# Kernel optimization log

Measured on AMD Instinct MI355X. Metric: run time of the kernel, lower is better.

Reference implementation:

```python
import jax, jax.numpy as jnp
import numpy as np

K = 3
NUM_STEP_COMBO = 5
BN_EPS = 1e-5


def setup_inputs() -> dict:
    key = jax.random.key(0)
    ks = jax.random.split(key, 10)
    N, E, D, H, O, G = 100000, 1600000, 48, 128, 12, 64
    x = jax.random.normal(ks[0], (N, D), dtype=jnp.float32)
    edge_index = jax.random.randint(ks[1], (2, E), 0, N, dtype=jnp.int64)
    batch = jnp.sort(jax.random.randint(ks[2], (N,), 0, G, dtype=jnp.int64))
    # ChebConv params: one [D, D] weight per Chebyshev order, shared bias
    W = jax.random.normal(ks[3], (K, D, D), dtype=jnp.float32) * 0.1
    b = jnp.zeros((D,), dtype=jnp.float32)
    gamma = jnp.ones((D,), dtype=jnp.float32)
    beta = jnp.zeros((D,), dtype=jnp.float32)
    W1 = jax.random.normal(ks[4], (D, H), dtype=jnp.float32) * 0.1
    b1 = jnp.zeros((H,), dtype=jnp.float32)
    W2 = jax.random.normal(ks[5], (H, O), dtype=jnp.float32) * 0.1
    b2 = jnp.zeros((O,), dtype=jnp.float32)
    return {"x": x, "edge_index": edge_index, "batch": batch, "num_graphs": 64,
            "W": W, "b": b, "gamma": gamma, "beta": beta,
            "W1": W1, "b1": b1, "W2": W2, "b2": b2}


def cheb_conv(x, row, col, W, b):
    # PyG ChebConv, sym norm, lambda_max=2 => L_hat = -D^{-1/2} A D^{-1/2}
    N = x.shape[0]
    deg = jax.ops.segment_sum(jnp.ones_like(row, dtype=x.dtype), row, num_segments=N)
    dinv = jnp.where(deg > 0, jax.lax.rsqrt(jnp.maximum(deg, 1.0)), 0.0)
    norm = (-dinv[row] * dinv[col])[:, None]  # [E,1] edge weights of L_hat

    def lhat(v):  # sparse matvec: gather neighbors, scale, scatter-add
        return jax.ops.segment_sum(norm * v[col], row, num_segments=N)

    Tx0 = x
    Tx1 = lhat(x)
    out = Tx0 @ W[0] + Tx1 @ W[1]
    Txkm2, Txkm1 = Tx0, Tx1
    for k in range(2, W.shape[0]):
        Txk = 2.0 * lhat(Txkm1) - Txkm2
        out = out + Txk @ W[k]
        Txkm2, Txkm1 = Txkm1, Txk
    return out + b


def reference(x, edge_index, batch, num_graphs, W, b, gamma, beta, W1, b1, W2, b2):
    row, col = edge_index[0], edge_index[1]
    N = x.shape[0]
    out = x
    for _ in range(NUM_STEP_COMBO):
        t = jax.nn.relu(cheb_conv(out, row, col, W, b))
        # BatchNorm1d (training-mode stats over all nodes, biased var)
        mean = jnp.mean(t, axis=0)
        var = jnp.mean((t - mean) ** 2, axis=0)
        t = gamma * (t - mean) * jax.lax.rsqrt(var + BN_EPS) + beta
        # graph_max_pool: per-node max over incoming neighbor features
        m = jax.ops.segment_max(t[col], row, num_segments=N)
        out = jnp.where(jnp.isneginf(m), 0.0, m)  # empty segments -> 0
    g = jax.ops.segment_sum(out, batch, num_segments=num_graphs)  # global_add_pool
    h = jax.nn.relu(g @ W1 + b1)
    return h @ W2 + b2
```

## Files before the change

kernel.cpp:

```cpp
#include <hip/hip_runtime.h>
#include <hip/hip_bf16.h>

#define D 48
#define GNUM 64
#define HDIM 128
#define ODIM 12
#define BN_EPS 1e-5f

typedef _Float16 half2v __attribute__((ext_vector_type(2)));
typedef _Float16 half4v __attribute__((ext_vector_type(4)));
typedef _Float16 half8v __attribute__((ext_vector_type(8)));

#if __has_builtin(__builtin_amdgcn_fdot2)
#define FDOT2(a, b, c) __builtin_amdgcn_fdot2((a), (b), (c), false)
#else
#define FDOT2(a, b, c) ((c) + (float)(a)[0] * (float)(b)[0] + (float)(a)[1] * (float)(b)[1])
#endif


__global__ __launch_bounds__(256) void k_deg(const int* __restrict__ row, int* __restrict__ deg, int E) {
    int e = blockIdx.x * 256 + threadIdx.x;
    if (e < E) atomicAdd(&deg[row[e]], 1);
}

__global__ __launch_bounds__(256) void k_dinv(const int* __restrict__ deg, float* __restrict__ dinv, int N) {
    int i = blockIdx.x * 256 + threadIdx.x;
    if (i < N) dinv[i] = deg[i] > 0 ? rsqrtf((float)deg[i]) : 0.f;
}

__global__ __launch_bounds__(256) void k_scan1(const int* __restrict__ deg, int* __restrict__ incl,
                                               int* __restrict__ bsum, int N) {
    __shared__ int s[256];
    int i = blockIdx.x * 256 + threadIdx.x;
    s[threadIdx.x] = (i < N) ? deg[i] : 0;
    __syncthreads();
    for (int off = 1; off < 256; off <<= 1) {
        int t = (threadIdx.x >= off) ? s[threadIdx.x - off] : 0;
        __syncthreads();
        s[threadIdx.x] += t;
        __syncthreads();
    }
    if (i < N) incl[i] = s[threadIdx.x];
    if (threadIdx.x == 255) bsum[blockIdx.x] = s[255];
}

__global__ __launch_bounds__(512) void k_scan2(int* __restrict__ bsum, int nb) {
    __shared__ int s[512];
    int t = threadIdx.x;
    s[t] = (t < nb) ? bsum[t] : 0;
    __syncthreads();
    for (int off = 1; off < 512; off <<= 1) {
        int v = (t >= off) ? s[t - off] : 0;
        __syncthreads();
        s[t] += v;
        __syncthreads();
    }
    if (t < nb) bsum[t] = s[t];
}

__global__ __launch_bounds__(256) void k_scan3(const int* __restrict__ incl, const int* __restrict__ bsum,
                                               int* __restrict__ rowptr, int N) {
    int i = blockIdx.x * 256 + threadIdx.x;
    if (i < N) {
        int add = (blockIdx.x > 0) ? bsum[blockIdx.x - 1] : 0;
        rowptr[i + 1] = incl[i] + add;
    }
    if (i == 0) rowptr[0] = 0;
}

__global__ __launch_bounds__(256) void k_fill(const int* __restrict__ row, const int* __restrict__ col,
                                              const int* __restrict__ rowptr, int* __restrict__ fillc,
                                              int* __restrict__ ecol, int E) {
    int e = blockIdx.x * 256 + threadIdx.x;
    if (e < E) {
        int r = row[e], c = col[e];
        int p = rowptr[r] + atomicAdd(&fillc[r], 1);
        ecol[p] = c;
    }
}

__global__ __launch_bounds__(256) void k_cvt(const float* __restrict__ x, const float* __restrict__ dinv,
                                             _Float16* __restrict__ xh, _Float16* __restrict__ xs, int n4) {
    int i = blockIdx.x * 256 + threadIdx.x;
    if (i < n4) {
        int node = i / 12;
        float dv = dinv[node];
        float4 v = ((const float4*)x)[i];
        half4v h, hs;
        h.x = (_Float16)v.x; h.y = (_Float16)v.y; h.z = (_Float16)v.z; h.w = (_Float16)v.w;
        hs.x = (_Float16)(dv * v.x); hs.y = (_Float16)(dv * v.y);
        hs.z = (_Float16)(dv * v.z); hs.w = (_Float16)(dv * v.w);
        ((half4v*)xh)[i] = h;
        ((half4v*)xs)[i] = hs;
    }
}


__global__ __launch_bounds__(256) void k_lhat(const _Float16* __restrict__ curs, const int* __restrict__ rowptr,
                                              const int* __restrict__ ecol, const float* __restrict__ dinv,
                                              _Float16* __restrict__ tx1, _Float16* __restrict__ tx1s, int N) {
    int lane = threadIdx.x & 63;
    int i = (blockIdx.x * 256 + threadIdx.x) >> 6;
    if (i >= N) return;
    int q = lane & 7, slot = lane >> 3;
    int qc = q < 6 ? q : 5;
    int s = rowptr[i], e = rowptr[i + 1];
    float a[8] = {0.f, 0.f, 0.f, 0.f, 0.f, 0.f, 0.f, 0.f};
    int p = s + slot;
    for (; p + 8 < e; p += 16) {
        int ca = ecol[p], cb = ecol[p + 8];
        half8v ha = *(const half8v*)(curs + (size_t)ca * D + qc * 8);
        half8v hb = *(const half8v*)(curs + (size_t)cb * D + qc * 8);
#pragma unroll
        for (int j = 0; j < 8; ++j) a[j] += (float)ha[j] + (float)hb[j];
    }
    if (p < e) {
        int ca = ecol[p];
        half8v ha = *(const half8v*)(curs + (size_t)ca * D + qc * 8);
#pragma unroll
        for (int j = 0; j < 8; ++j) a[j] += (float)ha[j];
    }
#pragma unroll
    for (int j = 0; j < 8; ++j) {
        a[j] += __shfl_xor(a[j], 8);
        a[j] += __shfl_xor(a[j], 16);
        a[j] += __shfl_xor(a[j], 32);
    }
    if (lane < 6) {
        float di = dinv[i];
        half8v o, os;
#pragma unroll
        for (int j = 0; j < 8; ++j) {
            float t = -di * a[j];
            o[j] = (_Float16)t;
            os[j] = (_Float16)(di * t);
        }
        *(half8v*)(tx1 + (size_t)i * D + lane * 8) = o;
        *(half8v*)(tx1s + (size_t)i * D + lane * 8) = os;
    }
}

__global__ __launch_bounds__(256) void k_gather2(const _Float16* __restrict__ tx0, const _Float16* __restrict__ tx1s,
                                                 const int* __restrict__ rowptr, const int* __restrict__ ecol,
                                                 const float* __restrict__ dinv, _Float16* __restrict__ tx2, int N) {
    int lane = threadIdx.x & 63;
    int i = (blockIdx.x * 256 + threadIdx.x) >> 6;
    if (i >= N) return;
    int q = lane & 7, slot = lane >> 3;
    int qc = q < 6 ? q : 5;
    int s = rowptr[i], e = rowptr[i + 1];
    float a[8] = {0.f, 0.f, 0.f, 0.f, 0.f, 0.f, 0.f, 0.f};
    int p = s + slot;
    for (; p + 8 < e; p += 16) {
        int ca = ecol[p], cb = ecol[p + 8];
        half8v ha = *(const half8v*)(tx1s + (size_t)ca * D + qc * 8);
        half8v hb = *(const half8v*)(tx1s + (size_t)cb * D + qc * 8);
#pragma unroll
        for (int j = 0; j < 8; ++j) a[j] += (float)ha[j] + (float)hb[j];
    }
    if (p < e) {
        int ca = ecol[p];
        half8v ha = *(const half8v*)(tx1s + (size_t)ca * D + qc * 8);
#pragma unroll
        for (int j = 0; j < 8; ++j) a[j] += (float)ha[j];
    }
#pragma unroll
    for (int j = 0; j < 8; ++j) {
        a[j] += __shfl_xor(a[j], 8);
        a[j] += __shfl_xor(a[j], 16);
        a[j] += __shfl_xor(a[j], 32);
    }
    if (lane < 6) {
        float sc = -2.f * dinv[i];
        half8v h0 = *(const half8v*)(tx0 + (size_t)i * D + lane * 8);
        half8v o;
#pragma unroll
        for (int j = 0; j < 8; ++j) o[j] = (_Float16)(sc * a[j] - (float)h0[j]);
        *(half8v*)(tx2 + (size_t)i * D + lane * 8) = o;
    }
}


__global__ __launch_bounds__(256) void k_dense(const _Float16* __restrict__ tx0, const _Float16* __restrict__ tx1,
                                               const _Float16* __restrict__ tx2, const float* __restrict__ W,
                                               const float* __restrict__ b, _Float16* __restrict__ tbuf, int N) {
    __shared__ half2v WH2[72 * D];
    __shared__ float bL[D];
    for (int t = threadIdx.x; t < 72 * D; t += 256) {
        int kp = t / D, j = t % D;
        half2v w;
        w.x = (_Float16)W[(2 * kp) * D + j];
        w.y = (_Float16)W[(2 * kp + 1) * D + j];
        WH2[t] = w;
    }
    if (threadIdx.x < D) bL[threadIdx.x] = b[threadIdx.x];
    __syncthreads();

    int base = (blockIdx.x * 256 + threadIdx.x) * 2;
    if (base >= N) return;
    bool two = (base + 1) < N;

    const _Float16* rowsA[3] = {tx0 + (size_t)base * D, tx1 + (size_t)base * D, tx2 + (size_t)base * D};
    size_t off2 = two ? D : 0;

    float acc0[D], acc1[D];
#pragma unroll
    for (int j = 0; j < D; ++j) { acc0[j] = bL[j]; acc1[j] = bL[j]; }

    for (int s = 0; s < 3; ++s) {
        const half2v* xa = (const half2v*)rowsA[s];
        const half2v* xb = (const half2v*)(rowsA[s] + off2);
#pragma unroll 4
        for (int g = 0; g < 24; ++g) {
            half2v va = xa[g], vb = xb[g];
            int kp = s * 24 + g;
            const half8v* wr = (const half8v*)&WH2[kp * D];
#pragma unroll
            for (int jc = 0; jc < 12; ++jc) {
                half8v w = wr[jc];
                half2v w0; w0.x = w[0]; w0.y = w[1];
                half2v w1; w1.x = w[2]; w1.y = w[3];
                half2v w2; w2.x = w[4]; w2.y = w[5];
                half2v w3; w3.x = w[6]; w3.y = w[7];
                acc0[jc * 4 + 0] = FDOT2(va, w0, acc0[jc * 4 + 0]);
                acc0[jc * 4 + 1] = FDOT2(va, w1, acc0[jc * 4 + 1]);
                acc0[jc * 4 + 2] = FDOT2(va, w2, acc0[jc * 4 + 2]);
                acc0[jc * 4 + 3] = FDOT2(va, w3, acc0[jc * 4 + 3]);
                acc1[jc * 4 + 0] = FDOT2(vb, w0, acc1[jc * 4 + 0]);
                acc1[jc * 4 + 1] = FDOT2(vb, w1, acc1[jc * 4 + 1]);
                acc1[jc * 4 + 2] = FDOT2(vb, w2, acc1[jc * 4 + 2]);
                acc1[jc * 4 + 3] = FDOT2(vb, w3, acc1[jc * 4 + 3]);
            }
        }
    }

    _Float16* o0 = tbuf + (size_t)base * D;
#pragma unroll
    for (int jc = 0; jc < 12; ++jc) {
        half4v h;
        h.x = (_Float16)fmaxf(acc0[jc * 4 + 0], 0.f);
        h.y = (_Float16)fmaxf(acc0[jc * 4 + 1], 0.f);
        h.z = (_Float16)fmaxf(acc0[jc * 4 + 2], 0.f);
        h.w = (_Float16)fmaxf(acc0[jc * 4 + 3], 0.f);
        *(half4v*)(o0 + jc * 4) = h;
    }
    if (two) {
        _Float16* o1 = o0 + D;
#pragma unroll
        for (int jc = 0; jc < 12; ++jc) {
            half4v h;
            h.x = (_Float16)fmaxf(acc1[jc * 4 + 0], 0.f);
            h.y = (_Float16)fmaxf(acc1[jc * 4 + 1], 0.f);
            h.z = (_Float16)fmaxf(acc1[jc * 4 + 2], 0.f);
            h.w = (_Float16)fmaxf(acc1[jc * 4 + 3], 0.f);
            *(half4v*)(o1 + jc * 4) = h;
        }
    }
}


__global__ __launch_bounds__(256) void k_bnstat(const _Float16* __restrict__ tbuf, float* __restrict__ bnstats, int N) {
    __shared__ float red[2 * D];
    if (threadIdx.x < 2 * D) red[threadIdx.x] = 0.f;
    __syncthreads();
    int tid = blockIdx.x * 256 + threadIdx.x;
    int q = tid % 12;
    int n0 = tid / 12;
    int stride = (gridDim.x * 256) / 12;
    float s0 = 0, s1 = 0, s2 = 0, s3 = 0, q0 = 0, q1 = 0, q2 = 0, q3 = 0;
    for (int n = n0; n < N; n += stride) {
        half4v h = *(const half4v*)(tbuf + (size_t)n * D + q * 4);
        float f0 = (float)h.x, f1 = (float)h.y, f2 = (float)h.z, f3 = (float)h.w;
        s0 += f0; s1 += f1; s2 += f2; s3 += f3;
        q0 += f0 * f0; q1 += f1 * f1; q2 += f2 * f2; q3 += f3 * f3;
    }
    atomicAdd(&red[q * 4 + 0], s0); atomicAdd(&red[q * 4 + 1], s1);
    atomicAdd(&red[q * 4 + 2], s2); atomicAdd(&red[q * 4 + 3], s3);
    atomicAdd(&red[D + q * 4 + 0], q0); atomicAdd(&red[D + q * 4 + 1], q1);
    atomicAdd(&red[D + q * 4 + 2], q2); atomicAdd(&red[D + q * 4 + 3], q3);
    __syncthreads();
    if (threadIdx.x < 2 * D) atomicAdd(&bnstats[threadIdx.x], red[threadIdx.x]);
}

__global__ __launch_bounds__(64) void k_bnfin(float* __restrict__ bnstats, const float* __restrict__ gamma,
                                              const float* __restrict__ beta, float* __restrict__ ss, float Ninv) {
    int t = threadIdx.x;
    if (t < D) {
        float mean = bnstats[t] * Ninv;
        float var = bnstats[D + t] * Ninv - mean * mean;
        var = fmaxf(var, 0.f);
        float sc = gamma[t] * rsqrtf(var + BN_EPS);
        ss[t] = sc;
        ss[D + t] = beta[t] - mean * sc;
        bnstats[t] = 0.f;
        bnstats[D + t] = 0.f;
    }
}


__global__ __launch_bounds__(256) void k_pool(const _Float16* __restrict__ tbuf, const int* __restrict__ rowptr,
                                              const int* __restrict__ ecol, const float* __restrict__ ss,
                                              const float* __restrict__ dinv, _Float16* __restrict__ outh,
                                              _Float16* __restrict__ outs, int N) {
    int lane = threadIdx.x & 63;
    int i = (blockIdx.x * 256 + threadIdx.x) >> 6;
    if (i >= N) return;
    int q = lane & 7, slot = lane >> 3;
    int qc = q < 6 ? q : 5;
    int s = rowptr[i], e = rowptr[i + 1];
    float mx[8], mn[8];
#pragma unroll
    for (int j = 0; j < 8; ++j) { mx[j] = -3.4e38f; mn[j] = 3.4e38f; }
    int p = s + slot;
    for (; p + 8 < e; p += 16) {
        int ca = ecol[p], cb = ecol[p + 8];
        half8v ha = *(const half8v*)(tbuf + (size_t)ca * D + qc * 8);
        half8v hb = *(const half8v*)(tbuf + (size_t)cb * D + qc * 8);
#pragma unroll
        for (int j = 0; j < 8; ++j) {
            float fa = (float)ha[j], fb = (float)hb[j];
            mx[j] = fmaxf(mx[j], fmaxf(fa, fb));
            mn[j] = fminf(mn[j], fminf(fa, fb));
        }
    }
    if (p < e) {
        int ca = ecol[p];
        half8v ha = *(const half8v*)(tbuf + (size_t)ca * D + qc * 8);
#pragma unroll
        for (int j = 0; j < 8; ++j) {
            float fa = (float)ha[j];
            mx[j] = fmaxf(mx[j], fa);
            mn[j] = fminf(mn[j], fa);
        }
    }
#pragma unroll
    for (int j = 0; j < 8; ++j) {
        mx[j] = fmaxf(mx[j], __shfl_xor(mx[j], 8));
        mx[j] = fmaxf(mx[j], __shfl_xor(mx[j], 16));
        mx[j] = fmaxf(mx[j], __shfl_xor(mx[j], 32));
        mn[j] = fminf(mn[j], __shfl_xor(mn[j], 8));
        mn[j] = fminf(mn[j], __shfl_xor(mn[j], 16));
        mn[j] = fminf(mn[j], __shfl_xor(mn[j], 32));
    }
    if (lane < 6) {
        float di = dinv[i];
        half8v o, os;
        if (s == e) {
#pragma unroll
            for (int j = 0; j < 8; ++j) { o[j] = (_Float16)0.f; os[j] = (_Float16)0.f; }
        } else {
#pragma unroll
            for (int j = 0; j < 8; ++j) {
                float scj = ss[lane * 8 + j];
                float shj = ss[D + lane * 8 + j];
                float v = (scj >= 0.f) ? scj * mx[j] + shj : scj * mn[j] + shj;
                o[j] = (_Float16)v;
                os[j] = (_Float16)(di * v);
            }
        }
        *(half8v*)(outh + (size_t)i * D + lane * 8) = o;
        *(half8v*)(outs + (size_t)i * D + lane * 8) = os;
    }
}


__global__ __launch_bounds__(256) void k_gpool(const _Float16* __restrict__ outh, const int* __restrict__ batch,
                                               float* __restrict__ g, int N, int chunk) {
    int lane = threadIdx.x & 63;
    int wid = (blockIdx.x * 256 + threadIdx.x) >> 6;
    int start = wid * chunk;
    if (start >= N || lane >= 12) return;
    int end = start + chunk;
    if (end > N) end = N;
    int curb = batch[start];
    float a0 = 0.f, a1 = 0.f, a2 = 0.f, a3 = 0.f;
    for (int i = start; i < end; ++i) {
        int bi = batch[i];
        if (bi != curb) {
            atomicAdd(&g[curb * D + lane * 4 + 0], a0); atomicAdd(&g[curb * D + lane * 4 + 1], a1);
            atomicAdd(&g[curb * D + lane * 4 + 2], a2); atomicAdd(&g[curb * D + lane * 4 + 3], a3);
            curb = bi; a0 = a1 = a2 = a3 = 0.f;
        }
        half4v h = *(const half4v*)(outh + (size_t)i * D + lane * 4);
        a0 += (float)h.x; a1 += (float)h.y; a2 += (float)h.z; a3 += (float)h.w;
    }
    atomicAdd(&g[curb * D + lane * 4 + 0], a0); atomicAdd(&g[curb * D + lane * 4 + 1], a1);
    atomicAdd(&g[curb * D + lane * 4 + 2], a2); atomicAdd(&g[curb * D + lane * 4 + 3], a3);
}

__global__ __launch_bounds__(256) void k_mlp(const float* __restrict__ g, const float* __restrict__ W1,
                                             const float* __restrict__ b1, const float* __restrict__ W2,
                                             const float* __restrict__ b2, float* __restrict__ out) {
    __shared__ float gL[GNUM * D];
    __shared__ float hL[GNUM * HDIM];
    __shared__ float W1L[D * HDIM];
    int t = threadIdx.x;
    for (int i = t; i < GNUM * D; i += 256) gL[i] = g[i];
    for (int i = t; i < D * HDIM; i += 256) W1L[i] = W1[i];
    __syncthreads();
    for (int i = t; i < GNUM * HDIM; i += 256) {
        int gi = i >> 7, hj = i & 127;
        float a = b1[hj];
        for (int k = 0; k < D; ++k) a += gL[gi * D + k] * W1L[k * HDIM + hj];
        hL[i] = fmaxf(a, 0.f);
    }
    __syncthreads();
    for (int i = t; i < GNUM * ODIM; i += 256) {
        int gi = i / ODIM, oj = i % ODIM;
        float a = b2[oj];
        for (int k = 0; k < HDIM; ++k) a += hL[gi * HDIM + k] * W2[k * ODIM + oj];
        out[i] = a;
    }
}


extern "C" void kernel_launch(void* const* d_in, const int* in_sizes, int n_in,
                              void* d_out, int out_size, void* d_ws, size_t ws_size,
                              hipStream_t stream) {
    const float* x     = (const float*)d_in[0];
    const int*   ei    = (const int*)d_in[1];
    const int*   batch = (const int*)d_in[2];
    const float* W     = (const float*)d_in[4];
    const float* b     = (const float*)d_in[5];
    const float* gamma = (const float*)d_in[6];
    const float* beta  = (const float*)d_in[7];
    const float* W1    = (const float*)d_in[8];
    const float* b1    = (const float*)d_in[9];
    const float* W2    = (const float*)d_in[10];
    const float* b2    = (const float*)d_in[11];

    int N = in_sizes[0] / D;
    int E = in_sizes[1] / 2;
    const int* row = ei;
    const int* col = ei + E;

    char* w = (char*)d_ws;
    auto alloc = [&](size_t bytes) { char* p = w; w += (bytes + 255) & ~(size_t)255; return p; };
    int*       deg     = (int*)alloc((size_t)N * 4);
    float*     dinv    = (float*)alloc((size_t)N * 4);
    int*       fillc   = (int*)alloc((size_t)N * 4);
    int*       incl    = (int*)alloc((size_t)N * 4);
    int*       bsum    = (int*)alloc(4096);
    int*       rowptr  = (int*)alloc((size_t)(N + 1) * 4);
    int*       ecol    = (int*)alloc((size_t)E * 4);
    _Float16*  xh      = (_Float16*)alloc((size_t)N * D * 2 + 64);
    _Float16*  xs      = (_Float16*)alloc((size_t)N * D * 2 + 64);
    _Float16*  tx1h    = (_Float16*)alloc((size_t)N * D * 2 + 64);
    _Float16*  tx1s    = (_Float16*)alloc((size_t)N * D * 2 + 64);
    _Float16*  tx2h    = (_Float16*)alloc((size_t)N * D * 2 + 64);
    _Float16*  tbufh   = (_Float16*)alloc((size_t)N * D * 2 + 64);
    _Float16*  outh    = (_Float16*)alloc((size_t)N * D * 2 + 64);
    _Float16*  outs    = (_Float16*)alloc((size_t)N * D * 2 + 64);
    float*     bnstats = (float*)alloc(2 * D * 4);
    float*     ss      = (float*)alloc(2 * D * 4);
    float*     g       = (float*)alloc((size_t)GNUM * D * 4);

    hipMemsetAsync(deg, 0, (size_t)N * 4, stream);
    hipMemsetAsync(fillc, 0, (size_t)N * 4, stream);
    hipMemsetAsync(bnstats, 0, 2 * D * 4, stream);
    hipMemsetAsync(g, 0, (size_t)GNUM * D * 4, stream);

    int nbE = (E + 255) / 256;
    int nbN = (N + 255) / 256;

    k_deg<<<nbE, 256, 0, stream>>>(row, deg, E);
    k_dinv<<<nbN, 256, 0, stream>>>(deg, dinv, N);
    k_scan1<<<nbN, 256, 0, stream>>>(deg, incl, bsum, N);
    k_scan2<<<1, 512, 0, stream>>>(bsum, nbN);
    k_scan3<<<nbN, 256, 0, stream>>>(incl, bsum, rowptr, N);
    k_fill<<<nbE, 256, 0, stream>>>(row, col, rowptr, fillc, ecol, E);
    int n4 = N * D / 4;
    k_cvt<<<(n4 + 255) / 256, 256, 0, stream>>>(x, dinv, xh, xs, n4);

    int nbWave = (N * 64 + 255) / 256;
    int nbDense = ((N + 1) / 2 + 255) / 256;
    const _Float16* curh = xh;
    const _Float16* curs = xs;
    for (int step = 0; step < 5; ++step) {
        k_lhat<<<nbWave, 256, 0, stream>>>(curs, rowptr, ecol, dinv, tx1h, tx1s, N);
        k_gather2<<<nbWave, 256, 0, stream>>>(curh, tx1s, rowptr, ecol, dinv, tx2h, N);
        k_dense<<<nbDense, 256, 0, stream>>>(curh, tx1h, tx2h, W, b, tbufh, N);
        k_bnstat<<<120, 256, 0, stream>>>(tbufh, bnstats, N);
        k_bnfin<<<1, 64, 0, stream>>>(bnstats, gamma, beta, ss, 1.f / (float)N);
        k_pool<<<nbWave, 256, 0, stream>>>(tbufh, rowptr, ecol, ss, dinv, outh, outs, N);
        curh = outh;
        curs = outs;
    }

    int chunk = 32;
    int nwaves = (N + chunk - 1) / chunk;
    int nbG = (nwaves * 64 + 255) / 256;
    k_gpool<<<nbG, 256, 0, stream>>>(outh, batch, g, N, chunk);
    k_mlp<<<1, 256, 0, stream>>>(g, W1, b1, W2, b2, (float*)d_out);
}
```

Baseline: 1.296 ms.

## Split feature arrays into three 16-channel planes and gather per plane

Result: slower. 2.338 ms (+80.4%).

```diff
diff --git a/kernel.cpp b/kernel.cpp
--- a/kernel.cpp
+++ b/kernel.cpp
@@ -80,110 +80,113 @@
 }
 
 __global__ __launch_bounds__(256) void k_cvt(const float* __restrict__ x, const float* __restrict__ dinv,
-                                             _Float16* __restrict__ xh, _Float16* __restrict__ xs, int n4) {
+                                             _Float16* __restrict__ xh, _Float16* __restrict__ xs,
+                                             int n4, size_t PS) {
     int i = blockIdx.x * 256 + threadIdx.x;
     if (i < n4) {
-        int node = i / 12;
+        int node = i / 12, fb = i % 12;
+        size_t dst = (size_t)(fb >> 2) * PS + (size_t)node * 16 + (fb & 3) * 4;
         float dv = dinv[node];
         float4 v = ((const float4*)x)[i];
         half4v h, hs;
         h.x = (_Float16)v.x; h.y = (_Float16)v.y; h.z = (_Float16)v.z; h.w = (_Float16)v.w;
         hs.x = (_Float16)(dv * v.x); hs.y = (_Float16)(dv * v.y);
         hs.z = (_Float16)(dv * v.z); hs.w = (_Float16)(dv * v.w);
-        ((half4v*)xh)[i] = h;
-        ((half4v*)xs)[i] = hs;
+        *(half4v*)(xh + dst) = h;
+        *(half4v*)(xs + dst) = hs;
     }
 }
 
 
 __global__ __launch_bounds__(256) void k_lhat(const _Float16* __restrict__ curs, const int* __restrict__ rowptr,
                                               const int* __restrict__ ecol, const float* __restrict__ dinv,
-                                              _Float16* __restrict__ tx1, _Float16* __restrict__ tx1s, int N) {
+                                              _Float16* __restrict__ tx1, _Float16* __restrict__ tx1s,
+                                              int N, int cc, size_t PS) {
     int lane = threadIdx.x & 63;
     int i = (blockIdx.x * 256 + threadIdx.x) >> 6;
     if (i >= N) return;
-    int q = lane & 7, slot = lane >> 3;
-    int qc = q < 6 ? q : 5;
+    int q = lane & 3, slot = lane >> 2;
+    const _Float16* plane = curs + (size_t)cc * PS;
     int s = rowptr[i], e = rowptr[i + 1];
-    float a[8] = {0.f, 0.f, 0.f, 0.f, 0.f, 0.f, 0.f, 0.f};
+    float a0 = 0.f, a1 = 0.f, a2 = 0.f, a3 = 0.f;
     int p = s + slot;
-    for (; p + 8 < e; p += 16) {
-        int ca = ecol[p], cb = ecol[p + 8];
-        half8v ha = *(const half8v*)(curs + (size_t)ca * D + qc * 8);
-        half8v hb = *(const half8v*)(curs + (size_t)cb * D + qc * 8);
-#pragma unroll
-        for (int j = 0; j < 8; ++j) a[j] += (float)ha[j] + (float)hb[j];
+    for (; p + 16 < e; p += 32) {
+        int ca = __builtin_nontemporal_load(ecol + p);
+        int cb = __builtin_nontemporal_load(ecol + p + 16);
+        half4v ha = *(const half4v*)(plane + (size_t)ca * 16 + q * 4);
+        half4v hb = *(const half4v*)(plane + (size_t)cb * 16 + q * 4);
+        a0 += (float)ha.x + (float)hb.x; a1 += (float)ha.y + (float)hb.y;
+        a2 += (float)ha.z + (float)hb.z; a3 += (float)ha.w + (float)hb.w;
     }
     if (p < e) {
-        int ca = ecol[p];
-        half8v ha = *(const half8v*)(curs + (size_t)ca * D + qc * 8);
-#pragma unroll
-        for (int j = 0; j < 8; ++j) a[j] += (float)ha[j];
-    }
-#pragma unroll
-    for (int j = 0; j < 8; ++j) {
-        a[j] += __shfl_xor(a[j], 8);
-        a[j] += __shfl_xor(a[j], 16);
-        a[j] += __shfl_xor(a[j], 32);
-    }
-    if (lane < 6) {
+        int ca = __builtin_nontemporal_load(ecol + p);
+        half4v ha = *(const half4v*)(plane + (size_t)ca * 16 + q * 4);
+        a0 += (float)ha.x; a1 += (float)ha.y; a2 += (float)ha.z; a3 += (float)ha.w;
+    }
+#pragma unroll
+    for (int m = 4; m <= 32; m <<= 1) {
+        a0 += __shfl_xor(a0, m); a1 += __shfl_xor(a1, m);
+        a2 += __shfl_xor(a2, m); a3 += __shfl_xor(a3, m);
+    }
+    if (slot == 0) {
         float di = dinv[i];
-        half8v o, os;
-#pragma unroll
-        for (int j = 0; j < 8; ++j) {
-            float t = -di * a[j];
-            o[j] = (_Float16)t;
-            os[j] = (_Float16)(di * t);
-        }
-        *(half8v*)(tx1 + (size_t)i * D + lane * 8) = o;
-        *(half8v*)(tx1s + (size_t)i * D + lane * 8) = os;
+        size_t dst = (size_t)cc * PS + (size_t)i * 16 + q * 4;
+        half4v o, os;
+        float t0 = -di * a0, t1 = -di * a1, t2 = -di * a2, t3 = -di * a3;
+        o.x = (_Float16)t0; o.y = (_Float16)t1; o.z = (_Float16)t2; o.w = (_Float16)t3;
+        os.x = (_Float16)(di * t0); os.y = (_Float16)(di * t1);
+        os.z = (_Float16)(di * t2); os.w = (_Float16)(di * t3);
+        *(half4v*)(tx1 + dst) = o;
+        *(half4v*)(tx1s + dst) = os;
     }
 }
 
 __global__ __launch_bounds__(256) void k_gather2(const _Float16* __restrict__ tx0, const _Float16* __restrict__ tx1s,
                                                  const int* __restrict__ rowptr, const int* __restrict__ ecol,
-                                                 const float* __restrict__ dinv, _Float16* __restrict__ tx2, int N) {
+                                                 const float* __restrict__ dinv, _Float16* __restrict__ tx2,
+                                                 int N, int cc, size_t PS) {
     int lane = threadIdx.x & 63;
     int i = (blockIdx.x * 256 + threadIdx.x) >> 6;
     if (i >= N) return;
-    int q = lane & 7, slot = lane >> 3;
-    int qc = q < 6 ? q : 5;
+    int q = lane & 3, slot = lane >> 2;
+    const _Float16* plane = tx1s + (size_t)cc * PS;
     int s = rowptr[i], e = rowptr[i + 1];
-    float a[8] = {0.f, 0.f, 0.f, 0.f, 0.f, 0.f, 0.f, 0.f};
+    float a0 = 0.f, a1 = 0.f, a2 = 0.f, a3 = 0.f;
     int p = s + slot;
-    for (; p + 8 < e; p += 16) {
-        int ca = ecol[p], cb = ecol[p + 8];
-        half8v ha = *(const half8v*)(tx1s + (size_t)ca * D + qc * 8);
-        half8v hb = *(const half8v*)(tx1s + (size_t)cb * D + qc * 8);
-#pragma unroll
-        for (int j = 0; j < 8; ++j) a[j] += (float)ha[j] + (float)hb[j];
+    for (; p + 16 < e; p += 32) {
+        int ca = __builtin_nontemporal_load(ecol + p);
+        int cb = __builtin_nontemporal_load(ecol + p + 16);
+        half4v ha = *(const half4v*)(plane + (size_t)ca * 16 + q * 4);
+        half4v hb = *(const half4v*)(plane + (size_t)cb * 16 + q * 4);
+        a0 += (float)ha.x + (float)hb.x; a1 += (float)ha.y + (float)hb.y;
+        a2 += (float)ha.z + (float)hb.z; a3 += (float)ha.w + (float)hb.w;
     }
     if (p < e) {
-        int ca = ecol[p];
-        half8v ha = *(const half8v*)(tx1s + (size_t)ca * D + qc * 8);
-#pragma unroll
-        for (int j = 0; j < 8; ++j) a[j] += (float)ha[j];
-    }
-#pragma unroll
-    for (int j = 0; j < 8; ++j) {
-        a[j] += __shfl_xor(a[j], 8);
-        a[j] += __shfl_xor(a[j], 16);
-        a[j] += __shfl_xor(a[j], 32);
-    }
-    if (lane < 6) {
+        int ca = __builtin_nontemporal_load(ecol + p);
+        half4v ha = *(const half4v*)(plane + (size_t)ca * 16 + q * 4);
+        a0 += (float)ha.x; a1 += (float)ha.y; a2 += (float)ha.z; a3 += (float)ha.w;
+    }
+#pragma unroll
+    for (int m = 4; m <= 32; m <<= 1) {
+        a0 += __shfl_xor(a0, m); a1 += __shfl_xor(a1, m);
+        a2 += __shfl_xor(a2, m); a3 += __shfl_xor(a3, m);
+    }
+    if (slot == 0) {
         float sc = -2.f * dinv[i];
-        half8v h0 = *(const half8v*)(tx0 + (size_t)i * D + lane * 8);
-        half8v o;
-#pragma unroll
-        for (int j = 0; j < 8; ++j) o[j] = (_Float16)(sc * a[j] - (float)h0[j]);
-        *(half8v*)(tx2 + (size_t)i * D + lane * 8) = o;
+        size_t dst = (size_t)cc * PS + (size_t)i * 16 + q * 4;
+        half4v h0 = *(const half4v*)(tx0 + dst);
+        half4v o;
+        o.x = (_Float16)(sc * a0 - (float)h0.x); o.y = (_Float16)(sc * a1 - (float)h0.y);
+        o.z = (_Float16)(sc * a2 - (float)h0.z); o.w = (_Float16)(sc * a3 - (float)h0.w);
+        *(half4v*)(tx2 + dst) = o;
     }
 }
 
 
 __global__ __launch_bounds__(256) void k_dense(const _Float16* __restrict__ tx0, const _Float16* __restrict__ tx1,
                                                const _Float16* __restrict__ tx2, const float* __restrict__ W,
-                                               const float* __restrict__ b, _Float16* __restrict__ tbuf, int N) {
+                                               const float* __restrict__ b, _Float16* __restrict__ tbuf,
+                                               int N, size_t PS) {
     __shared__ half2v WH2[72 * D];
     __shared__ float bL[D];
     for (int t = threadIdx.x; t < 72 * D; t += 256) {
@@ -199,67 +202,71 @@
     int base = (blockIdx.x * 256 + threadIdx.x) * 2;
     if (base >= N) return;
     bool two = (base + 1) < N;
-
-    const _Float16* rowsA[3] = {tx0 + (size_t)base * D, tx1 + (size_t)base * D, tx2 + (size_t)base * D};
-    size_t off2 = two ? D : 0;
+    int base2 = two ? base + 1 : base;
+
+    const _Float16* srcs[3] = {tx0, tx1, tx2};
 
     float acc0[D], acc1[D];
 #pragma unroll
     for (int j = 0; j < D; ++j) { acc0[j] = bL[j]; acc1[j] = bL[j]; }
 
     for (int s = 0; s < 3; ++s) {
-        const half2v* xa = (const half2v*)rowsA[s];
-        const half2v* xb = (const half2v*)(rowsA[s] + off2);
-#pragma unroll 4
-        for (int g = 0; g < 24; ++g) {
-            half2v va = xa[g], vb = xb[g];
-            int kp = s * 24 + g;
-            const half8v* wr = (const half8v*)&WH2[kp * D];
-#pragma unroll
-            for (int jc = 0; jc < 12; ++jc) {
-                half8v w = wr[jc];
-                half2v w0; w0.x = w[0]; w0.y = w[1];
-                half2v w1; w1.x = w[2]; w1.y = w[3];
-                half2v w2; w2.x = w[4]; w2.y = w[5];
-                half2v w3; w3.x = w[6]; w3.y = w[7];
-                acc0[jc * 4 + 0] = FDOT2(va, w0, acc0[jc * 4 + 0]);
-                acc0[jc * 4 + 1] = FDOT2(va, w1, acc0[jc * 4 + 1]);
-                acc0[jc * 4 + 2] = FDOT2(va, w2, acc0[jc * 4 + 2]);
-                acc0[jc * 4 + 3] = FDOT2(va, w3, acc0[jc * 4 + 3]);
-                acc1[jc * 4 + 0] = FDOT2(vb, w0, acc1[jc * 4 + 0]);
-                acc1[jc * 4 + 1] = FDOT2(vb, w1, acc1[jc * 4 + 1]);
-                acc1[jc * 4 + 2] = FDOT2(vb, w2, acc1[jc * 4 + 2]);
-                acc1[jc * 4 + 3] = FDOT2(vb, w3, acc1[jc * 4 + 3]);
+        const _Float16* tp = srcs[s];
+        for (int c = 0; c < 3; ++c) {
+            const half2v* xa = (const half2v*)(tp + (size_t)c * PS + (size_t)base * 16);
+            const half2v* xb = (const half2v*)(tp + (size_t)c * PS + (size_t)base2 * 16);
+#pragma unroll
+            for (int gg = 0; gg < 8; ++gg) {
+                half2v va = xa[gg], vb = xb[gg];
+                int kp = s * 24 + c * 8 + gg;
+                const half8v* wr = (const half8v*)&WH2[kp * D];
+#pragma unroll
+                for (int jc = 0; jc < 12; ++jc) {
+                    half8v w = wr[jc];
+                    half2v w0; w0.x = w[0]; w0.y = w[1];
+                    half2v w1; w1.x = w[2]; w1.y = w[3];
+                    half2v w2; w2.x = w[4]; w2.y = w[5];
+                    half2v w3; w3.x = w[6]; w3.y = w[7];
+                    acc0[jc * 4 + 0] = FDOT2(va, w0, acc0[jc * 4 + 0]);
+                    acc0[jc * 4 + 1] = FDOT2(va, w1, acc0[jc * 4 + 1]);
+                    acc0[jc * 4 + 2] = FDOT2(va, w2, acc0[jc * 4 + 2]);
+                    acc0[jc * 4 + 3] = FDOT2(va, w3, acc0[jc * 4 + 3]);
+                    acc1[jc * 4 + 0] = FDOT2(vb, w0, acc1[jc * 4 + 0]);
+                    acc1[jc * 4 + 1] = FDOT2(vb, w1, acc1[jc * 4 + 1]);
+                    acc1[jc * 4 + 2] = FDOT2(vb, w2, acc1[jc * 4 + 2]);
+                    acc1[jc * 4 + 3] = FDOT2(vb, w3, acc1[jc * 4 + 3]);
+                }
             }
         }
     }
 
-    _Float16* o0 = tbuf + (size_t)base * D;
 #pragma unroll
     for (int jc = 0; jc < 12; ++jc) {
+        size_t dst = (size_t)(jc >> 2) * PS + (size_t)base * 16 + (jc & 3) * 4;
         half4v h;
         h.x = (_Float16)fmaxf(acc0[jc * 4 + 0], 0.f);
         h.y = (_Float16)fmaxf(acc0[jc * 4 + 1], 0.f);
         h.z = (_Float16)fmaxf(acc0[jc * 4 + 2], 0.f);
         h.w = (_Float16)fmaxf(acc0[jc * 4 + 3], 0.f);
-        *(half4v*)(o0 + jc * 4) = h;
+        *(half4v*)(tbuf + dst) = h;
     }
     if (two) {
-        _Float16* o1 = o0 + D;
 #pragma unroll
         for (int jc = 0; jc < 12; ++jc) {
+            size_t dst = (size_t)(jc >> 2) * PS + (size_t)(base + 1) * 16 + (jc & 3) * 4;
             half4v h;
             h.x = (_Float16)fmaxf(acc1[jc * 4 + 0], 0.f);
             h.y = (_Float16)fmaxf(acc1[jc * 4 + 1], 0.f);
             h.z = (_Float16)fmaxf(acc1[jc * 4 + 2], 0.f);
             h.w = (_Float16)fmaxf(acc1[jc * 4 + 3], 0.f);
-            *(half4v*)(o1 + jc * 4) = h;
+            *(half4v*)(tbuf + dst) = h;
         }
     }
 }
 
 
-__global__ __launch_bounds__(256) void k_bnstat(const _Float16* __restrict__ tbuf, float* __restrict__ bnstats, int N) {
+__global__ __launch_bounds__(256) void k_bnstat(const _Float16* __restrict__ tbuf, float* __restrict__ bnstats,
+                                                int N, size_t PS) {
     __shared__ float red[2 * D];
     if (threadIdx.x < 2 * D) red[threadIdx.x] = 0.f;
     __syncthreads();
@@ -267,9 +274,10 @@
     int q = tid % 12;
     int n0 = tid / 12;
     int stride = (gridDim.x * 256) / 12;
+    size_t poff = (size_t)(q >> 2) * PS + (q & 3) * 4;
     float s0 = 0, s1 = 0, s2 = 0, s3 = 0, q0 = 0, q1 = 0, q2 = 0, q3 = 0;
     for (int n = n0; n < N; n += stride) {
-        half4v h = *(const half4v*)(tbuf + (size_t)n * D + q * 4);
+        half4v h = *(const half4v*)(tbuf + poff + (size_t)n * 16);
         float f0 = (float)h.x, f1 = (float)h.y, f2 = (float)h.z, f3 = (float)h.w;
         s0 += f0; s1 += f1; s2 += f2; s3 += f3;
         q0 += f0 * f0; q1 += f1 * f1; q2 += f2 * f2; q3 += f3 * f3;
@@ -301,77 +309,75 @@
 __global__ __launch_bounds__(256) void k_pool(const _Float16* __restrict__ tbuf, const int* __restrict__ rowptr,
                                               const int* __restrict__ ecol, const float* __restrict__ ss,
                                               const float* __restrict__ dinv, _Float16* __restrict__ outh,
-                                              _Float16* __restrict__ outs, int N) {
+                                              _Float16* __restrict__ outs, int N, int cc, size_t PS) {
     int lane = threadIdx.x & 63;
     int i = (blockIdx.x * 256 + threadIdx.x) >> 6;
     if (i >= N) return;
-    int q = lane & 7, slot = lane >> 3;
-    int qc = q < 6 ? q : 5;
+    int q = lane & 3, slot = lane >> 2;
+    const _Float16* plane = tbuf + (size_t)cc * PS;
     int s = rowptr[i], e = rowptr[i + 1];
-    float mx[8], mn[8];
-#pragma unroll
-    for (int j = 0; j < 8; ++j) { mx[j] = -3.4e38f; mn[j] = 3.4e38f; }
+    float m0 = -3.4e38f, m1 = -3.4e38f, m2 = -3.4e38f, m3 = -3.4e38f;
+    float n0 = 3.4e38f, n1 = 3.4e38f, n2 = 3.4e38f, n3 = 3.4e38f;
     int p = s + slot;
-    for (; p + 8 < e; p += 16) {
-        int ca = ecol[p], cb = ecol[p + 8];
-        half8v ha = *(const half8v*)(tbuf + (size_t)ca * D + qc * 8);
-        half8v hb = *(const half8v*)(tbuf + (size_t)cb * D + qc * 8);
-#pragma unroll
-        for (int j = 0; j < 8; ++j) {
-            float fa = (float)ha[j], fb = (float)hb[j];
-            mx[j] = fmaxf(mx[j], fmaxf(fa, fb));
-            mn[j] = fminf(mn[j], fminf(fa, fb));
+    for (; p + 16 < e; p += 32) {
+        int ca = __builtin_nontemporal_load(ecol + p);
+        int cb = __builtin_nontemporal_load(ecol + p + 16);
+        half4v ha = *(const half4v*)(plane + (size_t)ca * 16 + q * 4);
+        half4v hb = *(const half4v*)(plane + (size_t)cb * 16 + q * 4);
+        float fa0 = (float)ha.x, fa1 = (float)ha.y, fa2 = (float)ha.z, fa3 = (float)ha.w;
+        float fb0 = (float)hb.x, fb1 = (float)hb.y, fb2 = (float)hb.z, fb3 = (float)hb.w;
+        m0 = fmaxf(m0, fmaxf(fa0, fb0)); m1 = fmaxf(m1, fmaxf(fa1, fb1));
+        m2 = fmaxf(m2, fmaxf(fa2, fb2)); m3 = fmaxf(m3, fmaxf(fa3, fb3));
+        n0 = fminf(n0, fminf(fa0, fb0)); n1 = fminf(n1, fminf(fa1, fb1));
+        n2 = fminf(n2, fminf(fa2, fb2)); n3 = fminf(n3, fminf(fa3, fb3));
+    }
+    if (p < e) {
+        int ca = __builtin_nontemporal_load(ecol + p);
+        half4v ha = *(const half4v*)(plane + (size_t)ca * 16 + q * 4);
+        float fa0 = (float)ha.x, fa1 = (float)ha.y, fa2 = (float)ha.z, fa3 = (float)ha.w;
+        m0 = fmaxf(m0, fa0); m1 = fmaxf(m1, fa1); m2 = fmaxf(m2, fa2); m3 = fmaxf(m3, fa3);
+        n0 = fminf(n0, fa0); n1 = fminf(n1, fa1); n2 = fminf(n2, fa2); n3 = fminf(n3, fa3);
+    }
+#pragma unroll
+    for (int m = 4; m <= 32; m <<= 1) {
+        m0 = fmaxf(m0, __shfl_xor(m0, m)); m1 = fmaxf(m1, __shfl_xor(m1, m));
+        m2 = fmaxf(m2, __shfl_xor(m2, m)); m3 = fmaxf(m3, __shfl_xor(m3, m));
+        n0 = fminf(n0, __shfl_xor(n0, m)); n1 = fminf(n1, __shfl_xor(n1, m));
+        n2 = fminf(n2, __shfl_xor(n2, m)); n3 = fminf(n3, __shfl_xor(n3, m));
+    }
+    if (slot == 0) {
+        size_t dst = (size_t)cc * PS + (size_t)i * 16 + q * 4;
+        half4v o, os;
+        if (s == e) {
+            o.x = o.y = o.z = o.w = (_Float16)0.f;
+            os.x = os.y = os.z = os.w = (_Float16)0.f;
+        } else {
+            float di = dinv[i];
+            float4 sc = *(const float4*)(ss + cc * 16 + q * 4);
+            float4 sh = *(const float4*)(ss + D + cc * 16 + q * 4);
+            float v0 = (sc.x >= 0.f) ? sc.x * m0 + sh.x : sc.x * n0 + sh.x;
+            float v1 = (sc.y >= 0.f) ? sc.y * m1 + sh.y : sc.y * n1 + sh.y;
+            float v2 = (sc.z >= 0.f) ? sc.z * m2 + sh.z : sc.z * n2 + sh.z;
+            float v3 = (sc.w >= 0.f) ? sc.w * m3 + sh.w : sc.w * n3 + sh.w;
+            o.x = (_Float16)v0; o.y = (_Float16)v1; o.z = (_Float16)v2; o.w = (_Float16)v3;
+            os.x = (_Float16)(di * v0); os.y = (_Float16)(di * v1);
+            os.z = (_Float16)(di * v2); os.w = (_Float16)(di * v3);
         }
-    }
-    if (p < e) {
-        int ca = ecol[p];
-        half8v ha = *(const half8v*)(tbuf + (size_t)ca * D + qc * 8);
-#pragma unroll
-        for (int j = 0; j < 8; ++j) {
-            float fa = (float)ha[j];
-            mx[j] = fmaxf(mx[j], fa);
-            mn[j] = fminf(mn[j], fa);
-        }
-    }
-#pragma unroll
-    for (int j = 0; j < 8; ++j) {
-        mx[j] = fmaxf(mx[j], __shfl_xor(mx[j], 8));
-        mx[j] = fmaxf(mx[j], __shfl_xor(mx[j], 16));
-        mx[j] = fmaxf(mx[j], __shfl_xor(mx[j], 32));
-        mn[j] = fminf(mn[j], __shfl_xor(mn[j], 8));
-        mn[j] = fminf(mn[j], __shfl_xor(mn[j], 16));
-        mn[j] = fminf(mn[j], __shfl_xor(mn[j], 32));
-    }
-    if (lane < 6) {
-        float di = dinv[i];
-        half8v o, os;
-        if (s == e) {
-#pragma unroll
-            for (int j = 0; j < 8; ++j) { o[j] = (_Float16)0.f; os[j] = (_Float16)0.f; }
-        } else {
-#pragma unroll
-            for (int j = 0; j < 8; ++j) {
-                float scj = ss[lane * 8 + j];
-                float shj = ss[D + lane * 8 + j];
-                float v = (scj >= 0.f) ? scj * mx[j] + shj : scj * mn[j] + shj;
-                o[j] = (_Float16)v;
-                os[j] = (_Float16)(di * v);
-            }
-        }
-        *(half8v*)(outh + (size_t)i * D + lane * 8) = o;
-        *(half8v*)(outs + (size_t)i * D + lane * 8) = os;
+        *(half4v*)(outh + dst) = o;
+        *(half4v*)(outs + dst) = os;
     }
 }
 
 
 __global__ __launch_bounds__(256) void k_gpool(const _Float16* __restrict__ outh, const int* __restrict__ batch,
-                                               float* __restrict__ g, int N, int chunk) {
+                                               float* __restrict__ g, int N, int chunk, size_t PS) {
     int lane = threadIdx.x & 63;
     int wid = (blockIdx.x * 256 + threadIdx.x) >> 6;
     int start = wid * chunk;
     if (start >= N || lane >= 12) return;
     int end = start + chunk;
     if (end > N) end = N;
+    size_t poff = (size_t)(lane >> 2) * PS + (lane & 3) * 4;
     int curb = batch[start];
     float a0 = 0.f, a1 = 0.f, a2 = 0.f, a3 = 0.f;
     for (int i = start; i < end; ++i) {
@@ -381,7 +387,7 @@
             atomicAdd(&g[curb * D + lane * 4 + 2], a2); atomicAdd(&g[curb * D + lane * 4 + 3], a3);
             curb = bi; a0 = a1 = a2 = a3 = 0.f;
         }
-        half4v h = *(const half4v*)(outh + (size_t)i * D + lane * 4);
+        half4v h = *(const half4v*)(outh + poff + (size_t)i * 16);
         a0 += (float)h.x; a1 += (float)h.y; a2 += (float)h.z; a3 += (float)h.w;
     }
     atomicAdd(&g[curb * D + lane * 4 + 0], a0); atomicAdd(&g[curb * D + lane * 4 + 1], a1);
@@ -433,6 +439,7 @@
     int E = in_sizes[1] / 2;
     const int* row = ei;
     const int* col = ei + E;
+    size_t PS = (size_t)N * 16;
 
     char* w = (char*)d_ws;
     auto alloc = [&](size_t bytes) { char* p = w; w += (bytes + 255) & ~(size_t)255; return p; };
@@ -470,19 +477,22 @@
     k_scan3<<<nbN, 256, 0, stream>>>(incl, bsum, rowptr, N);
     k_fill<<<nbE, 256, 0, stream>>>(row, col, rowptr, fillc, ecol, E);
     int n4 = N * D / 4;
-    k_cvt<<<(n4 + 255) / 256, 256, 0, stream>>>(x, dinv, xh, xs, n4);
+    k_cvt<<<(n4 + 255) / 256, 256, 0, stream>>>(x, dinv, xh, xs, n4, PS);
 
     int nbWave = (N * 64 + 255) / 256;
     int nbDense = ((N + 1) / 2 + 255) / 256;
     const _Float16* curh = xh;
     const _Float16* curs = xs;
     for (int step = 0; step < 5; ++step) {
-        k_lhat<<<nbWave, 256, 0, stream>>>(curs, rowptr, ecol, dinv, tx1h, tx1s, N);
-        k_gather2<<<nbWave, 256, 0, stream>>>(curh, tx1s, rowptr, ecol, dinv, tx2h, N);
-        k_dense<<<nbDense, 256, 0, stream>>>(curh, tx1h, tx2h, W, b, tbufh, N);
-        k_bnstat<<<120, 256, 0, stream>>>(tbufh, bnstats, N);
+        for (int c = 0; c < 3; ++c)
+            k_lhat<<<nbWave, 256, 0, stream>>>(curs, rowptr, ecol, dinv, tx1h, tx1s, N, c, PS);
+        for (int c = 0; c < 3; ++c)
+            k_gather2<<<nbWave, 256, 0, stream>>>(curh, tx1s, rowptr, ecol, dinv, tx2h, N, c, PS);
+        k_dense<<<nbDense, 256, 0, stream>>>(curh, tx1h, tx2h, W, b, tbufh, N, PS);
+        k_bnstat<<<120, 256, 0, stream>>>(tbufh, bnstats, N, PS);
         k_bnfin<<<1, 64, 0, stream>>>(bnstats, gamma, beta, ss, 1.f / (float)N);
-        k_pool<<<nbWave, 256, 0, stream>>>(tbufh, rowptr, ecol, ss, dinv, outh, outs, N);
+        for (int c = 0; c < 3; ++c)
+            k_pool<<<nbWave, 256, 0, stream>>>(tbufh, rowptr, ecol, ss, dinv, outh, outs, N, c, PS);
         curh = outh;
         curs = outs;
     }
@@ -490,6 +500,6 @@
     int chunk = 32;
     int nwaves = (N + chunk - 1) / chunk;
     int nbG = (nwaves * 64 + 255) / 256;
-    k_gpool<<<nbG, 256, 0, stream>>>(outh, batch, g, N, chunk);
+    k_gpool<<<nbG, 256, 0, stream>>>(outh, batch, g, N, chunk, PS);
     k_mlp<<<1, 256, 0, stream>>>(g, W1, b1, W2, b2, (float*)d_out);
 }
```

## Bucket edges by row block for CSR fill, fold dinv and BN finalize

Applied to the files above, without the earlier changes.

Result: slower. 1.793 ms (+38.4%).

```diff
diff --git a/kernel.cpp b/kernel.cpp
--- a/kernel.cpp
+++ b/kernel.cpp
@@ -21,11 +21,6 @@
 __global__ __launch_bounds__(256) void k_deg(const int* __restrict__ row, int* __restrict__ deg, int E) {
     int e = blockIdx.x * 256 + threadIdx.x;
     if (e < E) atomicAdd(&deg[row[e]], 1);
-}
-
-__global__ __launch_bounds__(256) void k_dinv(const int* __restrict__ deg, float* __restrict__ dinv, int N) {
-    int i = blockIdx.x * 256 + threadIdx.x;
-    if (i < N) dinv[i] = deg[i] > 0 ? rsqrtf((float)deg[i]) : 0.f;
 }
 
 __global__ __launch_bounds__(256) void k_scan1(const int* __restrict__ deg, int* __restrict__ incl,
@@ -68,23 +63,43 @@
     if (i == 0) rowptr[0] = 0;
 }
 
-__global__ __launch_bounds__(256) void k_fill(const int* __restrict__ row, const int* __restrict__ col,
-                                              const int* __restrict__ rowptr, int* __restrict__ fillc,
-                                              int* __restrict__ ecol, int E) {
+__global__ __launch_bounds__(256) void k_bucket(const int* __restrict__ row, const int* __restrict__ col,
+                                                int* __restrict__ btail, int2* __restrict__ bstore,
+                                                int E, int CAP) {
     int e = blockIdx.x * 256 + threadIdx.x;
     if (e < E) {
         int r = row[e], c = col[e];
-        int p = rowptr[r] + atomicAdd(&fillc[r], 1);
-        ecol[p] = c;
-    }
-}
-
-__global__ __launch_bounds__(256) void k_cvt(const float* __restrict__ x, const float* __restrict__ dinv,
-                                             _Float16* __restrict__ xh, _Float16* __restrict__ xs, int n4) {
+        int b = r >> 8;
+        int t = atomicAdd(&btail[b], 1);
+        if (t < CAP) bstore[(size_t)b * CAP + t] = make_int2(r, c);
+    }
+}
+
+__global__ __launch_bounds__(256) void k_fill2(const int2* __restrict__ bstore, const int* __restrict__ btail,
+                                               const int* __restrict__ rowptr, int* __restrict__ ecol, int CAP) {
+    __shared__ int cnt[256];
+    int b = blockIdx.x;
+    cnt[threadIdx.x] = 0;
+    __syncthreads();
+    int tcnt = btail[b];
+    if (tcnt > CAP) tcnt = CAP;
+    const int2* src = bstore + (size_t)b * CAP;
+    for (int t = threadIdx.x; t < tcnt; t += 256) {
+        int2 e = src[t];
+        int k = atomicAdd(&cnt[e.x & 255], 1);
+        ecol[rowptr[e.x] + k] = e.y;
+    }
+}
+
+__global__ __launch_bounds__(256) void k_cvt(const float* __restrict__ x, const int* __restrict__ deg,
+                                             _Float16* __restrict__ xh, _Float16* __restrict__ xs,
+                                             float* __restrict__ dinv, int n4) {
     int i = blockIdx.x * 256 + threadIdx.x;
     if (i < n4) {
         int node = i / 12;
-        float dv = dinv[node];
+        int dg = deg[node];
+        float dv = dg > 0 ? rsqrtf((float)dg) : 0.f;
+        if (i % 12 == 0) dinv[node] = dv;
         float4 v = ((const float4*)x)[i];
         half4v h, hs;
         h.x = (_Float16)v.x; h.y = (_Float16)v.y; h.z = (_Float16)v.z; h.w = (_Float16)v.w;
@@ -259,8 +274,12 @@
 }
 
 
-__global__ __launch_bounds__(256) void k_bnstat(const _Float16* __restrict__ tbuf, float* __restrict__ bnstats, int N) {
+__global__ __launch_bounds__(256) void k_bnstat(const _Float16* __restrict__ tbuf, float* __restrict__ bnstats,
+                                                const float* __restrict__ gamma, const float* __restrict__ beta,
+                                                float* __restrict__ ss, int* __restrict__ done,
+                                                float Ninv, int N) {
     __shared__ float red[2 * D];
+    __shared__ int isLast;
     if (threadIdx.x < 2 * D) red[threadIdx.x] = 0.f;
     __syncthreads();
     int tid = blockIdx.x * 256 + threadIdx.x;
@@ -280,20 +299,27 @@
     atomicAdd(&red[D + q * 4 + 2], q2); atomicAdd(&red[D + q * 4 + 3], q3);
     __syncthreads();
     if (threadIdx.x < 2 * D) atomicAdd(&bnstats[threadIdx.x], red[threadIdx.x]);
-}
-
-__global__ __launch_bounds__(64) void k_bnfin(float* __restrict__ bnstats, const float* __restrict__ gamma,
-                                              const float* __restrict__ beta, float* __restrict__ ss, float Ninv) {
-    int t = threadIdx.x;
-    if (t < D) {
-        float mean = bnstats[t] * Ninv;
-        float var = bnstats[D + t] * Ninv - mean * mean;
-        var = fmaxf(var, 0.f);
-        float sc = gamma[t] * rsqrtf(var + BN_EPS);
-        ss[t] = sc;
-        ss[D + t] = beta[t] - mean * sc;
-        bnstats[t] = 0.f;
-        bnstats[D + t] = 0.f;
+    __threadfence();
+    if (threadIdx.x == 0) {
+        int old = atomicAdd(done, 1);
+        isLast = (old == (int)gridDim.x - 1);
+    }
+    __syncthreads();
+    if (isLast) {
+        __threadfence();
+        if (threadIdx.x < D) {
+            volatile float* vb = bnstats;
+            int t = threadIdx.x;
+            float mean = vb[t] * Ninv;
+            float var = vb[D + t] * Ninv - mean * mean;
+            var = fmaxf(var, 0.f);
+            float sc = gamma[t] * rsqrtf(var + BN_EPS);
+            ss[t] = sc;
+            ss[D + t] = beta[t] - mean * sc;
+            bnstats[t] = 0.f;
+            bnstats[D + t] = 0.f;
+            if (t == 0) atomicExch(done, 0);
+        }
     }
 }
 
@@ -434,15 +460,19 @@
     const int* row = ei;
     const int* col = ei + E;
 
+    int NBUCK = (N + 255) >> 8;
+    int CAP = E / NBUCK + 2048;
+
     char* w = (char*)d_ws;
     auto alloc = [&](size_t bytes) { char* p = w; w += (bytes + 255) & ~(size_t)255; return p; };
     int*       deg     = (int*)alloc((size_t)N * 4);
     float*     dinv    = (float*)alloc((size_t)N * 4);
-    int*       fillc   = (int*)alloc((size_t)N * 4);
     int*       incl    = (int*)alloc((size_t)N * 4);
     int*       bsum    = (int*)alloc(4096);
     int*       rowptr  = (int*)alloc((size_t)(N + 1) * 4);
     int*       ecol    = (int*)alloc((size_t)E * 4);
+    int*       btail   = (int*)alloc((size_t)NBUCK * 4);
+    int2*      bstore  = (int2*)alloc((size_t)NBUCK * CAP * 8);
     _Float16*  xh      = (_Float16*)alloc((size_t)N * D * 2 + 64);
     _Float16*  xs      = (_Float16*)alloc((size_t)N * D * 2 + 64);
     _Float16*  tx1h    = (_Float16*)alloc((size_t)N * D * 2 + 64);
@@ -453,35 +483,36 @@
     _Float16*  outs    = (_Float16*)alloc((size_t)N * D * 2 + 64);
     float*     bnstats = (float*)alloc(2 * D * 4);
     float*     ss      = (float*)alloc(2 * D * 4);
+    int*       done    = (int*)alloc(256);
     float*     g       = (float*)alloc((size_t)GNUM * D * 4);
 
     hipMemsetAsync(deg, 0, (size_t)N * 4, stream);
-    hipMemsetAsync(fillc, 0, (size_t)N * 4, stream);
+    hipMemsetAsync(btail, 0, (size_t)NBUCK * 4, stream);
     hipMemsetAsync(bnstats, 0, 2 * D * 4, stream);
+    hipMemsetAsync(done, 0, 256, stream);
     hipMemsetAsync(g, 0, (size_t)GNUM * D * 4, stream);
 
     int nbE = (E + 255) / 256;
     int nbN = (N + 255) / 256;
 
     k_deg<<<nbE, 256, 0, stream>>>(row, deg, E);
-    k_dinv<<<nbN, 256, 0, stream>>>(deg, dinv, N);
     k_scan1<<<nbN, 256, 0, stream>>>(deg, incl, bsum, N);
     k_scan2<<<1, 512, 0, stream>>>(bsum, nbN);
     k_scan3<<<nbN, 256, 0, stream>>>(incl, bsum, rowptr, N);
-    k_fill<<<nbE, 256, 0, stream>>>(row, col, rowptr, fillc, ecol, E);
+    k_bucket<<<nbE, 256, 0, stream>>>(row, col, btail, bstore, E, CAP);
+    k_fill2<<<NBUCK, 256, 0, stream>>>(bstore, btail, rowptr, ecol, CAP);
     int n4 = N * D / 4;
-    k_cvt<<<(n4 + 255) / 256, 256, 0, stream>>>(x, dinv, xh, xs, n4);
+    k_cvt<<<(n4 + 255) / 256, 256, 0, stream>>>(x, deg, xh, xs, dinv, n4);
 
     int nbWave = (N * 64 + 255) / 256;
-    int nbDense = ((N + 1) / 2 + 255) / 256;
+    int nbDense = (((N + 1) / 2) + 255) / 256;
     const _Float16* curh = xh;
     const _Float16* curs = xs;
     for (int step = 0; step < 5; ++step) {
         k_lhat<<<nbWave, 256, 0, stream>>>(curs, rowptr, ecol, dinv, tx1h, tx1s, N);
         k_gather2<<<nbWave, 256, 0, stream>>>(curh, tx1s, rowptr, ecol, dinv, tx2h, N);
         k_dense<<<nbDense, 256, 0, stream>>>(curh, tx1h, tx2h, W, b, tbufh, N);
-        k_bnstat<<<120, 256, 0, stream>>>(tbufh, bnstats, N);
-        k_bnfin<<<1, 64, 0, stream>>>(bnstats, gamma, beta, ss, 1.f / (float)N);
+        k_bnstat<<<120, 256, 0, stream>>>(tbufh, bnstats, gamma, beta, ss, done, 1.f / (float)N, N);
         k_pool<<<nbWave, 256, 0, stream>>>(tbufh, rowptr, ecol, ss, dinv, outh, outs, N);
         curh = outh;
         curs = outs;
```
